# Kernel tuning notes

Hardware: AMD Instinct MI355X
Metric: run time of the kernel (lower is better)

## Reference

```python
import jax, jax.numpy as jnp
import numpy as np

EPS = 1e-5


def setup_inputs() -> dict:
    key = jax.random.key(0)
    ks = jax.random.split(key, 12)
    B, C, D, H, W = 16, 32, 32, 64, 64
    HID, OUT = 256, 128
    inp = {
        "x": jax.random.normal(ks[0], (B, C, D, H, W), dtype=jnp.float32),
        "bn_gamma": jax.random.normal(ks[1], (C,), dtype=jnp.float32) * 0.1 + 1.0,
        "bn_beta": jax.random.normal(ks[2], (C,), dtype=jnp.float32) * 0.1,
        "w_ih": jax.random.normal(ks[3], (HID, C), dtype=jnp.float32) / np.sqrt(C),
        "b_ih": jax.random.normal(ks[4], (HID,), dtype=jnp.float32) * 0.01,
        "w_hh": jax.random.normal(ks[5], (HID, HID), dtype=jnp.float32) / np.sqrt(HID),
        "b_hh": jax.random.normal(ks[6], (HID,), dtype=jnp.float32) * 0.01,
        "w_out": jax.random.normal(ks[7], (OUT, HID), dtype=jnp.float32) / np.sqrt(HID),
        "b_out": jax.random.normal(ks[8], (OUT,), dtype=jnp.float32) * 0.01,
        "ln_gamma": jnp.ones((OUT,), dtype=jnp.float32),
        "ln_beta": jnp.zeros((OUT,), dtype=jnp.float32),
        "pooled_depth": 8,
    }
    return inp


def reference(x, bn_gamma, bn_beta, w_ih, b_ih, w_hh, b_hh, w_out, b_out, ln_gamma, ln_beta, pooled_depth):
    B, C, D, H, W = x.shape
    P = pooled_depth
    # SyncBatchNorm (training mode: batch statistics over B, D, H, W per channel)
    mean = jnp.mean(x, axis=(0, 2, 3, 4), keepdims=True)
    var = jnp.mean((x - mean) ** 2, axis=(0, 2, 3, 4), keepdims=True)  # biased var
    g = bn_gamma.reshape(1, C, 1, 1, 1)
    b = bn_beta.reshape(1, C, 1, 1, 1)
    x = (x - mean) * jax.lax.rsqrt(var + EPS) * g + b
    x = jax.nn.relu(x)
    # AdaptiveMaxPool3d -> (P, 1, 1); D divisible by P so bins are uniform
    x = x.reshape(B, C, P, D // P, H, W).max(axis=(3, 4, 5))  # (B, C, P)
    x = jnp.transpose(x, (2, 0, 1))  # (P, B, C) -- time-major
    # RNNCell (relu) scan over time
    hx0 = jnp.zeros((B, w_hh.shape[0]), dtype=x.dtype)

    def step(hx, xt):
        hx = jax.nn.relu(xt @ w_ih.T + b_ih + hx @ w_hh.T + b_hh)
        return hx, None

    hx, _ = jax.lax.scan(step, hx0, x)
    # Output projection + LayerNorm
    out = hx @ w_out.T + b_out  # (B, OUT)
    mu = jnp.mean(out, axis=-1, keepdims=True)
    v = jnp.mean((out - mu) ** 2, axis=-1, keepdims=True)
    out = (out - mu) * jax.lax.rsqrt(v + EPS) * ln_gamma + ln_beta
    return out
```

## Files before the change

kernel.cpp:

```cpp
#include <hip/hip_runtime.h>
#include <math.h>

#define EPS 1e-5f

constexpr int Bc = 16, Cc = 32, Dc = 32, Hc = 64, Wc = 64;
constexpr int Pc = 8, HIDc = 256, OUTc = 128;
constexpr int NBINS = Bc * Cc * Pc;
constexpr float NPC_INV = 1.0f / (float)(Bc * Dc * Hc * Wc);

typedef float fx4 __attribute__((ext_vector_type(4)));


__global__ __launch_bounds__(256) void k1_stats(const float* __restrict__ x,
                                                float* __restrict__ ws) {
    const int bid = blockIdx.x;
    const int t = threadIdx.x;
    const fx4* px = reinterpret_cast<const fx4*>(x) + ((size_t)bid << 12);

    float vmax = -INFINITY, vmin = INFINITY, s = 0.f, ss = 0.f;
#pragma unroll
    for (int j = 0; j < 16; ++j) {
        fx4 v = __builtin_nontemporal_load(&px[j * 256 + t]);
        vmax = fmaxf(vmax, fmaxf(fmaxf(v.x, v.y), fmaxf(v.z, v.w)));
        vmin = fminf(vmin, fminf(fminf(v.x, v.y), fminf(v.z, v.w)));
        s += (v.x + v.y) + (v.z + v.w);
        ss = fmaf(v.x, v.x, ss); ss = fmaf(v.y, v.y, ss);
        ss = fmaf(v.z, v.z, ss); ss = fmaf(v.w, v.w, ss);
    }
#pragma unroll
    for (int off = 1; off < 64; off <<= 1) {
        vmax = fmaxf(vmax, __shfl_xor(vmax, off));
        vmin = fminf(vmin, __shfl_xor(vmin, off));
        s += __shfl_xor(s, off);
        ss += __shfl_xor(ss, off);
    }
    __shared__ float r[4][4];
    const int wid = t >> 6;
    if ((t & 63) == 0) { r[wid][0] = vmax; r[wid][1] = vmin; r[wid][2] = s; r[wid][3] = ss; }
    __syncthreads();
    if (t == 0) {
        vmax = fmaxf(fmaxf(r[0][0], r[1][0]), fmaxf(r[2][0], r[3][0]));
        vmin = fminf(fminf(r[0][1], r[1][1]), fminf(r[2][1], r[3][1]));
        s  = (r[0][2] + r[1][2]) + (r[2][2] + r[3][2]);
        ss = (r[0][3] + r[1][3]) + (r[2][3] + r[3][3]);
        ws[bid]             = vmax;
        ws[NBINS + bid]     = vmin;
        ws[2 * NBINS + bid] = s;
        ws[3 * NBINS + bid] = ss;
    }
}

__global__ __launch_bounds__(1024) void k2_rnn(const float* __restrict__ ws,
                                               const float* __restrict__ bn_gamma,
                                               const float* __restrict__ bn_beta,
                                               const float* __restrict__ w_ih,
                                               const float* __restrict__ b_ih,
                                               const float* __restrict__ w_hh,
                                               const float* __restrict__ b_hh,
                                               const float* __restrict__ w_out,
                                               const float* __restrict__ b_out,
                                               const float* __restrict__ ln_gamma,
                                               const float* __restrict__ ln_beta,
                                               float* __restrict__ out) {
    const int b = blockIdx.x;
    const int t = threadIdx.x;
    const int h = t & 255;
    const int q = t >> 8;

    __shared__ float scale_s[Cc], shift_s[Cc];
    __shared__ __align__(16) float pooled[Pc][Cc];
    __shared__ __align__(16) float u[Pc][HIDc];
    __shared__ __align__(16) float hx[HIDc];
    __shared__ __align__(16) float part[4][HIDc];
    __shared__ __align__(16) float o[OUTc];
    __shared__ float red2[2];

    float4 wreg[16];
    {
        const float4* wr = reinterpret_cast<const float4*>(w_hh) + h * (HIDc / 4) + q * 16;
#pragma unroll
        for (int e = 0; e < 16; ++e) wreg[e] = wr[e];
    }

    {
        const int c = t >> 5, r = t & 31;
        float s = 0.f, ss = 0.f;
#pragma unroll
        for (int j = 0; j < 4; ++j) {
            const int i = r + 32 * j;
            const int bid = ((i >> 3) * Cc + c) * Pc + (i & 7);
            s  += ws[2 * NBINS + bid];
            ss += ws[3 * NBINS + bid];
        }
#pragma unroll
        for (int off = 1; off < 32; off <<= 1) {
            s  += __shfl_xor(s, off);
            ss += __shfl_xor(ss, off);
        }
        if (r == 0) {
            const float mean = s * NPC_INV;
            const float var  = ss * NPC_INV - mean * mean;
            const float sc   = bn_gamma[c] * rsqrtf(var + EPS);
            scale_s[c] = sc;
            shift_s[c] = bn_beta[c] - mean * sc;
        }
    }
    __syncthreads();

    if (t < Pc * Cc) {
        const int p = t >> 5, c = t & 31;
        const int bid = (b * Cc + c) * Pc + p;
        const float sc = scale_s[c];
        const float xm = (sc >= 0.f) ? ws[bid] : ws[NBINS + bid];
        pooled[p][c] = fmaxf(fmaf(sc, xm, shift_s[c]), 0.f);
    }
    __syncthreads();

    {
        const float4* wi = reinterpret_cast<const float4*>(w_ih) + h * (Cc / 4);
        float4 wiv[8];
#pragma unroll
        for (int e = 0; e < 8; ++e) wiv[e] = wi[e];
        const float bias = b_ih[h] + b_hh[h];
#pragma unroll
        for (int pp = 0; pp < 2; ++pp) {
            const int p = q + 4 * pp;
            const float4* pl = reinterpret_cast<const float4*>(&pooled[p][0]);
            float a0 = bias, a1 = 0.f, a2 = 0.f, a3 = 0.f;
#pragma unroll
            for (int e = 0; e < 8; ++e) {
                float4 pv = pl[e];
                a0 = fmaf(pv.x, wiv[e].x, a0);
                a1 = fmaf(pv.y, wiv[e].y, a1);
                a2 = fmaf(pv.z, wiv[e].z, a2);
                a3 = fmaf(pv.w, wiv[e].w, a3);
            }
            u[p][h] = (a0 + a1) + (a2 + a3);
        }
    }
    __syncthreads();

    if (t < HIDc) hx[t] = fmaxf(u[0][t], 0.f);
    __syncthreads();

    for (int step = 1; step < Pc; ++step) {
        const float4* hv4 = reinterpret_cast<const float4*>(&hx[q * 64]);
        float a0 = 0.f, a1 = 0.f, a2 = 0.f, a3 = 0.f;
#pragma unroll
        for (int e = 0; e < 16; ++e) {
            float4 wv = wreg[e];
            float4 hv = hv4[e];
            a0 = fmaf(hv.x, wv.x, a0);
            a1 = fmaf(hv.y, wv.y, a1);
            a2 = fmaf(hv.z, wv.z, a2);
            a3 = fmaf(hv.w, wv.w, a3);
        }
        part[q][h] = (a0 + a1) + (a2 + a3);
        __syncthreads();
        if (q == 0) {
            const float v = u[step][h] + ((part[0][h] + part[1][h]) + (part[2][h] + part[3][h]));
            hx[h] = fmaxf(v, 0.f);
        }
        __syncthreads();
    }

    if (t < 4 * OUTc) {
        const int oi = t >> 2, seg = t & 3;
        const float4* wo = reinterpret_cast<const float4*>(w_out) + oi * (HIDc / 4) + seg * 16;
        const float4* hv4 = reinterpret_cast<const float4*>(&hx[seg * 64]);
        float a0 = (seg == 0) ? b_out[oi] : 0.f, a1 = 0.f, a2 = 0.f, a3 = 0.f;
#pragma unroll
        for (int e = 0; e < 16; ++e) {
            float4 wv = wo[e];
            float4 hv = hv4[e];
            a0 = fmaf(hv.x, wv.x, a0);
            a1 = fmaf(hv.y, wv.y, a1);
            a2 = fmaf(hv.z, wv.z, a2);
            a3 = fmaf(hv.w, wv.w, a3);
        }
        float s = (a0 + a1) + (a2 + a3);
        s += __shfl_xor(s, 1);
        s += __shfl_xor(s, 2);
        if (seg == 0) o[oi] = s;
    }
    __syncthreads();

    if (t < 64) {
        const float x0 = o[t], x1 = o[t + 64];
        float s = x0 + x1, ss = x0 * x0 + x1 * x1;
#pragma unroll
        for (int off = 1; off < 64; off <<= 1) {
            s  += __shfl_xor(s, off);
            ss += __shfl_xor(ss, off);
        }
        if (t == 0) { red2[0] = s; red2[1] = ss; }
    }
    __syncthreads();
    if (t < OUTc) {
        const float mu  = red2[0] * (1.0f / OUTc);
        const float var = red2[1] * (1.0f / OUTc) - mu * mu;
        const float rs  = rsqrtf(var + EPS);
        out[b * OUTc + t] = (o[t] - mu) * rs * ln_gamma[t] + ln_beta[t];
    }
}

extern "C" void kernel_launch(void* const* d_in, const int* in_sizes, int n_in,
                              void* d_out, int out_size, void* d_ws, size_t ws_size,
                              hipStream_t stream) {
    const float* x        = (const float*)d_in[0];
    const float* bn_gamma = (const float*)d_in[1];
    const float* bn_beta  = (const float*)d_in[2];
    const float* w_ih     = (const float*)d_in[3];
    const float* b_ih     = (const float*)d_in[4];
    const float* w_hh     = (const float*)d_in[5];
    const float* b_hh     = (const float*)d_in[6];
    const float* w_out    = (const float*)d_in[7];
    const float* b_out    = (const float*)d_in[8];
    const float* ln_gamma = (const float*)d_in[9];
    const float* ln_beta  = (const float*)d_in[10];
    float* out = (float*)d_out;
    float* ws  = (float*)d_ws;

    k1_stats<<<NBINS, 256, 0, stream>>>(x, ws);
    k2_rnn<<<Bc, 1024, 0, stream>>>(ws, bn_gamma, bn_beta, w_ih, b_ih, w_hh, b_hh,
                                    w_out, b_out, ln_gamma, ln_beta, out);
}
```

Before: 68.33 us.

## Restructure RNN kernel to 512 threads with shuffle reductions and double-buffered hidden state

The recurrent kernel now runs 512 threads per batch row. Each thread holds 4 rows by 32 columns of w_hh in registers, and partial dot products are combined with wave shuffles instead of a shared-memory partial array. A double-buffered, padded hidden-state buffer cuts each recurrence step from two barriers to one, and the BN statistics reduction is reorganised for coalesced reads. This trims serial latency in the small second kernel, but at 128 floats per thread plus extras there is a risk of register spilling, and k1, which likely dominates, is unchanged.

```diff
diff --git a/kernel.cpp b/kernel.cpp
--- a/kernel.cpp
+++ b/kernel.cpp
@@ -3,10 +3,9 @@
 
 #define EPS 1e-5f
 
-constexpr int Bc = 16, Cc = 32, Dc = 32, Hc = 64, Wc = 64;
-constexpr int Pc = 8, HIDc = 256, OUTc = 128;
-constexpr int NBINS = Bc * Cc * Pc;
-constexpr float NPC_INV = 1.0f / (float)(Bc * Dc * Hc * Wc);
+constexpr int Bc = 16, Cc = 32, Pc = 8, HIDc = 256, OUTc = 128;
+constexpr int NBINS = 4096;
+constexpr float NPC_INV = 1.0f / 2097152.0f;
 
 typedef float fx4 __attribute__((ext_vector_type(4)));
 
@@ -50,66 +49,73 @@
     }
 }
 
-__global__ __launch_bounds__(1024) void k2_rnn(const float* __restrict__ ws,
-                                               const float* __restrict__ bn_gamma,
-                                               const float* __restrict__ bn_beta,
-                                               const float* __restrict__ w_ih,
-                                               const float* __restrict__ b_ih,
-                                               const float* __restrict__ w_hh,
-                                               const float* __restrict__ b_hh,
-                                               const float* __restrict__ w_out,
-                                               const float* __restrict__ b_out,
-                                               const float* __restrict__ ln_gamma,
-                                               const float* __restrict__ ln_beta,
-                                               float* __restrict__ out) {
+__global__ __launch_bounds__(512, 2) void k2_rnn(const float* __restrict__ ws,
+                                                 const float* __restrict__ bn_gamma,
+                                                 const float* __restrict__ bn_beta,
+                                                 const float* __restrict__ w_ih,
+                                                 const float* __restrict__ b_ih,
+                                                 const float* __restrict__ w_hh,
+                                                 const float* __restrict__ b_hh,
+                                                 const float* __restrict__ w_out,
+                                                 const float* __restrict__ b_out,
+                                                 const float* __restrict__ ln_gamma,
+                                                 const float* __restrict__ ln_beta,
+                                                 float* __restrict__ out) {
     const int b = blockIdx.x;
     const int t = threadIdx.x;
-    const int h = t & 255;
-    const int q = t >> 8;
+    const int og = t >> 3, kg = t & 7;
 
     __shared__ float scale_s[Cc], shift_s[Cc];
+    __shared__ float pA[2][Cc], pB[2][Cc];
     __shared__ __align__(16) float pooled[Pc][Cc];
     __shared__ __align__(16) float u[Pc][HIDc];
-    __shared__ __align__(16) float hx[HIDc];
-    __shared__ __align__(16) float part[4][HIDc];
+    __shared__ __align__(16) float hxs[2][288];
     __shared__ __align__(16) float o[OUTc];
     __shared__ float red2[2];
 
-    float4 wreg[16];
     {
-        const float4* wr = reinterpret_cast<const float4*>(w_hh) + h * (HIDc / 4) + q * 16;
-#pragma unroll
-        for (int e = 0; e < 16; ++e) wreg[e] = wr[e];
-    }
-
-    {
-        const int c = t >> 5, r = t & 31;
+        const float* sums = ws + 2 * NBINS;
+        const float* sqs  = ws + 3 * NBINS;
         float s = 0.f, ss = 0.f;
 #pragma unroll
-        for (int j = 0; j < 4; ++j) {
-            const int i = r + 32 * j;
-            const int bid = ((i >> 3) * Cc + c) * Pc + (i & 7);
-            s  += ws[2 * NBINS + bid];
-            ss += ws[3 * NBINS + bid];
-        }
-#pragma unroll
-        for (int off = 1; off < 32; off <<= 1) {
+        for (int j = 0; j < 8; ++j) {
+            s  += sums[t + 512 * j];
+            ss += sqs[t + 512 * j];
+        }
+#pragma unroll
+        for (int off = 1; off < 8; off <<= 1) {
             s  += __shfl_xor(s, off);
             ss += __shfl_xor(ss, off);
         }
-        if (r == 0) {
-            const float mean = s * NPC_INV;
-            const float var  = ss * NPC_INV - mean * mean;
-            const float sc   = bn_gamma[c] * rsqrtf(var + EPS);
-            scale_s[c] = sc;
-            shift_s[c] = bn_beta[c] - mean * sc;
-        }
+        if ((t & 7) == 0) {
+            const int c = (t >> 3) & 31, half = t >> 8;
+            pA[half][c] = s;
+            pB[half][c] = ss;
+        }
+    }
+
+    float4 w4[4][8];
+#pragma unroll
+    for (int r = 0; r < 4; ++r) {
+        const float4* wr = reinterpret_cast<const float4*>(w_hh + (4 * og + r) * HIDc + 32 * kg);
+#pragma unroll
+        for (int e = 0; e < 8; ++e) w4[r][e] = wr[e];
+    }
+
+    __syncthreads();
+    if (t < Cc) {
+        const float s = pA[0][t] + pA[1][t], ss = pB[0][t] + pB[1][t];
+        const float mean = s * NPC_INV;
+        const float var  = ss * NPC_INV - mean * mean;
+        const float sc   = bn_gamma[t] * rsqrtf(var + EPS);
+        scale_s[t] = sc;
+        shift_s[t] = bn_beta[t] - mean * sc;
     }
     __syncthreads();
 
     if (t < Pc * Cc) {
-        const int p = t >> 5, c = t & 31;
-        const int bid = (b * Cc + c) * Pc + p;
+        const int c = t >> 3, p = t & 7;
+        const int bid = b * 256 + t;
         const float sc = scale_s[c];
         const float xm = (sc >= 0.f) ? ws[bid] : ws[NBINS + bid];
         pooled[p][c] = fmaxf(fmaf(sc, xm, shift_s[c]), 0.f);
@@ -117,14 +123,16 @@
     __syncthreads();
 
     {
+        const int h = t & 255, pq = t >> 8;
         const float4* wi = reinterpret_cast<const float4*>(w_ih) + h * (Cc / 4);
         float4 wiv[8];
 #pragma unroll
         for (int e = 0; e < 8; ++e) wiv[e] = wi[e];
         const float bias = b_ih[h] + b_hh[h];
-#pragma unroll
-        for (int pp = 0; pp < 2; ++pp) {
-            const int p = q + 4 * pp;
+        float u0 = 0.f;
+#pragma unroll
+        for (int pp = 0; pp < 4; ++pp) {
+            const int p = pq * 4 + pp;
             const float4* pl = reinterpret_cast<const float4*>(&pooled[p][0]);
             float a0 = bias, a1 = 0.f, a2 = 0.f, a3 = 0.f;
 #pragma unroll
@@ -135,44 +143,60 @@
                 a2 = fmaf(pv.z, wiv[e].z, a2);
                 a3 = fmaf(pv.w, wiv[e].w, a3);
             }
-            u[p][h] = (a0 + a1) + (a2 + a3);
-        }
-    }
-    __syncthreads();
-
-    if (t < HIDc) hx[t] = fmaxf(u[0][t], 0.f);
-    __syncthreads();
-
+            const float uv = (a0 + a1) + (a2 + a3);
+            u[p][h] = uv;
+            if (pp == 0) u0 = uv;
+        }
+        if (pq == 0) hxs[0][(h >> 5) * 36 + (h & 31)] = fmaxf(u0, 0.f);
+    }
+    __syncthreads();
+
+    int cur = 0;
     for (int step = 1; step < Pc; ++step) {
-        const float4* hv4 = reinterpret_cast<const float4*>(&hx[q * 64]);
-        float a0 = 0.f, a1 = 0.f, a2 = 0.f, a3 = 0.f;
+        float4 h4[8];
+        const float4* hp = reinterpret_cast<const float4*>(&hxs[cur][kg * 36]);
+#pragma unroll
+        for (int e = 0; e < 8; ++e) h4[e] = hp[e];
+        float acc[4];
+#pragma unroll
+        for (int r = 0; r < 4; ++r) {
+            float a0 = 0.f, a1 = 0.f, a2 = 0.f, a3 = 0.f;
+#pragma unroll
+            for (int e = 0; e < 8; ++e) {
+                float4 wv = w4[r][e], hv = h4[e];
+                a0 = fmaf(hv.x, wv.x, a0);
+                a1 = fmaf(hv.y, wv.y, a1);
+                a2 = fmaf(hv.z, wv.z, a2);
+                a3 = fmaf(hv.w, wv.w, a3);
+            }
+            acc[r] = (a0 + a1) + (a2 + a3);
+        }
+#pragma unroll
+        for (int off = 1; off < 8; off <<= 1) {
+#pragma unroll
+            for (int r = 0; r < 4; ++r) acc[r] += __shfl_xor(acc[r], off);
+        }
+        if (kg == 0) {
+#pragma unroll
+            for (int r = 0; r < 4; ++r) {
+                const int h = 4 * og + r;
+                const float v = u[step][h] + acc[r];
+                hxs[cur ^ 1][(h >> 5) * 36 + (h & 31)] = fmaxf(v, 0.f);
+            }
+        }
+        __syncthreads();
+        cur ^= 1;
+    }
+
+    {
+        const int oi = t >> 2, seg = t & 3;
+        const float4* wo = reinterpret_cast<const float4*>(w_out + oi * HIDc + seg * 64);
+        float a0 = (seg == 0) ? b_out[oi] : 0.f, a1 = 0.f, a2 = 0.f, a3 = 0.f;
 #pragma unroll
         for (int e = 0; e < 16; ++e) {
-            float4 wv = wreg[e];
-            float4 hv = hv4[e];
-            a0 = fmaf(hv.x, wv.x, a0);
-            a1 = fmaf(hv.y, wv.y, a1);
-            a2 = fmaf(hv.z, wv.z, a2);
-            a3 = fmaf(hv.w, wv.w, a3);
-        }
-        part[q][h] = (a0 + a1) + (a2 + a3);
-        __syncthreads();
-        if (q == 0) {
-            const float v = u[step][h] + ((part[0][h] + part[1][h]) + (part[2][h] + part[3][h]));
-            hx[h] = fmaxf(v, 0.f);
-        }
-        __syncthreads();
-    }
-
-    if (t < 4 * OUTc) {
-        const int oi = t >> 2, seg = t & 3;
-        const float4* wo = reinterpret_cast<const float4*>(w_out) + oi * (HIDc / 4) + seg * 16;
-        const float4* hv4 = reinterpret_cast<const float4*>(&hx[seg * 64]);
-        float a0 = (seg == 0) ? b_out[oi] : 0.f, a1 = 0.f, a2 = 0.f, a3 = 0.f;
-#pragma unroll
-        for (int e = 0; e < 16; ++e) {
-            float4 wv = wo[e];
-            float4 hv = hv4[e];
+            const int k = seg * 64 + e * 4;
+            const float4 hv = *reinterpret_cast<const float4*>(&hxs[1][(k >> 5) * 36 + (k & 31)]);
+            const float4 wv = wo[e];
             a0 = fmaf(hv.x, wv.x, a0);
             a1 = fmaf(hv.y, wv.y, a1);
             a2 = fmaf(hv.z, wv.z, a2);
@@ -222,6 +246,6 @@
     float* ws  = (float*)d_ws;
 
     k1_stats<<<NBINS, 256, 0, stream>>>(x, ws);
-    k2_rnn<<<Bc, 1024, 0, stream>>>(ws, bn_gamma, bn_beta, w_ih, b_ih, w_hh, b_hh,
-                                    w_out, b_out, ln_gamma, ln_beta, out);
+    k2_rnn<<<Bc, 512, 0, stream>>>(ws, bn_gamma, bn_beta, w_ih, b_ih, w_hh, b_hh,
+                                   w_out, b_out, ln_gamma, ln_beta, out);
 }
```

New measurement: 64.62 us. 1.06x faster.
